# Performance work log

Measured on AMD Instinct MI355X. Metric: run time of the kernel, lower is better.

The kernel has to match this reference:

```python
import jax, jax.numpy as jnp
import numpy as np

C_RGLRU = 8.0

def _rg_lru(x, wa, ba, wx, bx, lam):
    # x: [B, L, D]. Griffin RG-LRU (De et al. 2024).
    r = jax.nn.sigmoid(jnp.einsum('bld,ed->ble', x, wa) + ba)
    i = jax.nn.sigmoid(jnp.einsum('bld,ed->ble', x, wx) + bx)
    log_a = -C_RGLRU * r * jax.nn.softplus(lam)          # [B,L,D], <= 0
    a = jnp.exp(log_a)
    mult = jnp.sqrt(jnp.maximum(1.0 - jnp.exp(2.0 * log_a), 0.0))
    b = mult * (i * x)
    def combine(c1, c2):
        a1, b1 = c1
        a2, b2 = c2
        return a1 * a2, a2 * b1 + b2
    _, h = jax.lax.associative_scan(combine, (a, b), axis=1)
    return h

def setup_inputs() -> dict:
    key = jax.random.key(0)
    ks = jax.random.split(key, 12)
    B, L, D, R = 4, 2048, 2048, 2560
    s_d = 1.0 / np.sqrt(D)
    s_r = 1.0 / np.sqrt(R)
    s_c = 1.0 / np.sqrt(R * 4)
    return {
        'x':      jax.random.normal(ks[0], (B, L, D), jnp.float32),
        'w1':     jax.random.normal(ks[1], (R, D), jnp.float32) * s_d,
        'b1':     jnp.zeros((R,), jnp.float32),
        'conv_w': jax.random.normal(ks[2], (R, R, 4), jnp.float32) * s_c,
        'conv_b': jnp.zeros((R,), jnp.float32),
        'wa':     jax.random.normal(ks[3], (R, R), jnp.float32) * s_r,
        'ba':     jnp.zeros((R,), jnp.float32),
        'wx':     jax.random.normal(ks[4], (R, R), jnp.float32) * s_r,
        'bx':     jnp.zeros((R,), jnp.float32),
        'lam':    jax.random.uniform(ks[5], (R,), jnp.float32, 0.5, 2.0),
        'w2':     jax.random.normal(ks[6], (D, R), jnp.float32) * s_r,
        'b2':     jnp.zeros((D,), jnp.float32),
    }

def reference(x, w1, b1, conv_w, conv_b, wa, ba, wx, bx, lam, w2, b2):
    # linear1 + SiLU: [B,L,D] -> [B,L,R]
    h = jax.nn.silu(jnp.einsum('bld,rd->blr', x, w1) + b1)
    # temporal conv1d: kernel 4, dilation 2, padding 3 both sides (as in torch)
    hc = h.transpose(0, 2, 1)  # [B,R,L]
    hc = jax.lax.conv_general_dilated(
        hc, conv_w, window_strides=(1,), padding=[(3, 3)],
        rhs_dilation=(2,), dimension_numbers=('NCH', 'OIH', 'NCH'))
    hc = hc + conv_b[None, :, None]
    h = hc.transpose(0, 2, 1)  # [B,L,R]
    # RG-LRU gated linear recurrence
    h = _rg_lru(h, wa, ba, wx, bx, lam)
    # linear2: [B,L,R] -> [B,L,D]
    return jnp.einsum('blr,dr->bld', h, w2) + b2
```

## Files before the change

kernel.cpp:

```cpp
#include <hip/hip_runtime.h>

#define B_  4
#define L_  2048
#define D_  2048
#define R_  2560
#define BL_ (B_ * L_)
#define LP_ (L_ + 6)

#define CHK_  16
#define CLEN_ (L_ / CHK_)

typedef unsigned short u16;
typedef unsigned int   u32;

typedef __attribute__((ext_vector_type(8))) short short8;
typedef __attribute__((ext_vector_type(4))) float f32x4;

static __device__ __forceinline__ u16 f2bf(float f) {
  u32 x = __float_as_uint(f);
  x += 0x7fffu + ((x >> 16) & 1u);
  return (u16)(x >> 16);
}
static __device__ __forceinline__ float bf2f(u16 u) {
  return __uint_as_float(((u32)u) << 16);
}

static __device__ __forceinline__ void gld16(const u16* g, u16* l) {
  __builtin_amdgcn_global_load_lds(
      (const __attribute__((address_space(1))) void*)g,
      (__attribute__((address_space(3))) void*)l, 16, 0, 0);
}

#define SB0()     __builtin_amdgcn_sched_barrier(0)
#define BAR()     __builtin_amdgcn_s_barrier()
#define LGKM0()   do { asm volatile("s_waitcnt lgkmcnt(0)" ::: "memory"); SB0(); } while (0)

__global__ void cvt_bf16(const float* __restrict__ src, u16* __restrict__ dst, int n) {
  int i = blockIdx.x * blockDim.x + threadIdx.x;
  int stride = gridDim.x * blockDim.x;
  for (; i < n; i += stride) dst[i] = f2bf(src[i]);
}

__global__ void cvt_convw(const float* __restrict__ cw, u16* __restrict__ out) {
  int i = blockIdx.x * blockDim.x + threadIdx.x;
  if (i >= R_ * R_) return;
  const float4 v = *(const float4*)(cw + (size_t)i * 4);
  out[(size_t)0 * R_ * R_ + i] = f2bf(v.x);
  out[(size_t)1 * R_ * R_ + i] = f2bf(v.y);
  out[(size_t)2 * R_ * R_ + i] = f2bf(v.z);
  out[(size_t)3 * R_ * R_ + i] = f2bf(v.w);
}

__global__ void zero_pads(u16* __restrict__ h1p) {
  int i = blockIdx.x * blockDim.x + threadIdx.x;
  if (i >= 24 * R_) return;
  const int rr = i / R_, c = i % R_;
  const int b = rr / 6, k = rr % 6;
  const int row = b * LP_ + (k < 3 ? k : L_ + k);
  h1p[(size_t)row * R_ + c] = 0;
}

__global__ void cat_bias(const float* __restrict__ ba, const float* __restrict__ bx,
                         float* __restrict__ bcat) {
  int i = blockIdx.x * blockDim.x + threadIdx.x;
  if (i < R_) bcat[i] = ba[i];
  else if (i < 2 * R_) bcat[i] = bx[i - R_];
}

template <int NF, int IB>
__device__ __forceinline__ void mfma_block(f32x4 (&acc)[8][NF], const short8 (&aF)[4],
                                           const short8 (&bF)[NF]) {
#pragma unroll
  for (int i = 0; i < 4; ++i)
#pragma unroll
    for (int j = 0; j < NF; ++j)
      acc[IB + i][j] =
          __builtin_amdgcn_mfma_f32_16x16x32_bf16(aF[i], bF[j], acc[IB + i][j], 0, 0, 0);
}

template <int KDIM, int TAPS, int ACT, int OBF16, int PADOUT>
__global__ __launch_bounds__(512)
__attribute__((amdgpu_waves_per_eu(2, 2)))
void gemm256(const u16* __restrict__ A, const u16* __restrict__ Bm,
             const float* __restrict__ bias, void* __restrict__ Cv, int N, int NBX) {
  constexpr int NF  = 4;
  constexpr int NTK = KDIM / 64;
  constexpr int NT  = NTK * TAPS;
  constexpr int BUFU16 = 16384 + NF * 4096;
  __shared__ u16 lds[2][BUFU16];

  const int cpx = gridDim.x >> 3;
  int lin = blockIdx.x;
  lin = (lin & 7) * cpx + (lin >> 3);
  const int bx = lin % NBX, by = lin / NBX;

  const int tid  = threadIdx.x;
  const int wave = tid >> 6, lane = tid & 63;
  const int wr = wave >> 2, wc = wave & 3;
  const int q = lane >> 4, r16 = lane & 15;
  const int rsw = r16 & 7;
  const int bm = bx * 256, bn = by * 256;
  const int srow = tid >> 3;
  const int schunk = (tid & 7) ^ (srow & 7);
  const int bbatch = bm >> 11;
  const int arow0 = (TAPS == 4) ? (bm + 3 + 6 * bbatch) : bm;

  f32x4 acc[8][NF] = {};

  auto stA = [&](int u, int h) {
    const int uc = (u < NT) ? u : (NT - 1);
    const int tap = uc / NTK;
    const int ku  = (uc % NTK) * 64;
    const int sh  = (TAPS == 4) ? (2 * tap - 3) : 0;
    const u16* src = A + (size_t)(arow0 + sh + h * 128) * KDIM + ku + schunk * 8;
    u16* dst = &lds[u & 1][h * 8192 + wave * 512];
#pragma unroll
    for (int s = 0; s < 2; ++s)
      gld16(src + (size_t)(s * 64 + srow) * KDIM, dst + s * 4096);
  };
  auto stB = [&](int u, int j) {
    const int uc = (u < NT) ? u : (NT - 1);
    const int tap = uc / NTK;
    const int ku  = (uc % NTK) * 64;
    const u16* src = Bm + (size_t)tap * R_ * R_ +
                     (size_t)(bn + j * 64 + srow) * KDIM + ku + schunk * 8;
    gld16(src, &lds[u & 1][16384 + j * 4096 + wave * 512]);
  };
  auto ldA = [&](short8 (&f)[4], int p, int half, int k) {
    const int base = half * 8192 + (wr * 64 + r16) * 64 + ((k * 4 + q) ^ rsw) * 8;
#pragma unroll
    for (int i = 0; i < 4; ++i)
      f[i] = *(const short8*)&lds[p][base + i * 1024];
  };
  auto ldB = [&](short8 (&f)[NF], int p, int k) {
    const int base = 16384 + (wc * 16 + r16) * 64 + ((k * 4 + q) ^ rsw) * 8;
#pragma unroll
    for (int j = 0; j < NF; ++j)
      f[j] = *(const short8*)&lds[p][base + j * 4096];
  };

  stA(0, 0); stA(0, 1);
#pragma unroll
  for (int j = 0; j < NF; ++j) stB(0, j);
  stA(1, 0);
#pragma unroll
  for (int j = 0; j < NF; ++j) stB(1, j);
  asm volatile("s_waitcnt vmcnt(%0)" :: "n"(NF + 2) : "memory");
  SB0();
  BAR();

  short8 aF[4], bF[NF];
  for (int t = 0; t < NT; ++t) {
    const int p = t & 1;
    ldA(aF, p, 0, 0);
    ldB(bF, p, 0);
    stA(t + 1, 1);
    BAR(); LGKM0();
    __builtin_amdgcn_s_setprio(1);
    mfma_block<NF, 0>(acc, aF, bF);
    __builtin_amdgcn_s_setprio(0);
    SB0(); BAR();
    ldA(aF, p, 1, 0);
    BAR(); LGKM0();
    __builtin_amdgcn_s_setprio(1);
    mfma_block<NF, 4>(acc, aF, bF);
    __builtin_amdgcn_s_setprio(0);
    SB0(); BAR();
    ldA(aF, p, 0, 1);
    ldB(bF, p, 1);
    BAR(); LGKM0();
    __builtin_amdgcn_s_setprio(1);
    mfma_block<NF, 0>(acc, aF, bF);
    __builtin_amdgcn_s_setprio(0);
    SB0(); BAR();
    ldA(aF, p, 1, 1);
    stA(t + 2, 0);
#pragma unroll
    for (int j = 0; j < NF; ++j) stB(t + 2, j);
    BAR(); LGKM0();
    __builtin_amdgcn_s_setprio(1);
    mfma_block<NF, 4>(acc, aF, bF);
    __builtin_amdgcn_s_setprio(0);
    asm volatile("s_waitcnt vmcnt(%0)" :: "n"(NF + 2) : "memory");
    SB0(); BAR();
  }

#pragma unroll
  for (int i = 0; i < 8; ++i) {
    const int rb  = ((i & 4) ? 128 : 0) + wr * 64 + (i & 3) * 16;
    const int row = bm + rb + q * 4;
    const int orow = PADOUT ? (row + 3 + 6 * bbatch) : row;
#pragma unroll
    for (int j = 0; j < NF; ++j) {
      const int col = bn + j * 64 + wc * 16 + r16;
      const float bv = bias[col];
#pragma unroll
      for (int rr = 0; rr < 4; ++rr) {
        float v = acc[i][j][rr] + bv;
        if (ACT == 1) v = v / (1.f + __expf(-v));
        const size_t off = (size_t)(orow + rr) * N + col;
        if (OBF16) ((u16*)Cv)[off] = f2bf(v);
        else       ((float*)Cv)[off] = v;
      }
    }
  }
}

static __device__ __forceinline__ void gate_math(u16 ga_, u16 gi_, u16 h2_, float sp,
                                                 float& a, float& b) {
  const float ga = bf2f(ga_);
  const float gi = bf2f(gi_);
  const float h2 = bf2f(h2_);
  const float rr = 1.f / (1.f + __expf(-ga));
  const float ii = 1.f / (1.f + __expf(-gi));
  const float log_a = -8.f * rr * sp;
  a = __expf(log_a);
  const float e2 = __expf(2.f * log_a);
  b = sqrtf(fmaxf(1.f - e2, 0.f)) * ii * h2;
}

__global__ void scan_pass1(const u16* __restrict__ gcat, const u16* __restrict__ h2b,
                           const float* __restrict__ lam,
                           float* __restrict__ Aprod, float* __restrict__ Hend) {
  int t = blockIdx.x * blockDim.x + threadIdx.x;
  if (t >= CHK_ * B_ * R_) return;
  const int c = t / (B_ * R_), br = t % (B_ * R_);
  const int b = br / R_, r = br % R_;
  const float sp = log1pf(__expf(lam[r]));
  size_t rowbase = (size_t)b * L_ + (size_t)c * CLEN_;
  const u16* pg  = gcat + rowbase * (2 * R_) + r;
  const u16* ph2 = h2b + rowbase * R_ + r;
  float Ap = 1.f, h = 0.f;
  for (int l = 0; l < CLEN_; ++l) {
    float a, bb;
    gate_math(pg[0], pg[R_], ph2[0], sp, a, bb);
    Ap *= a;
    h = a * h + bb;
    pg += 2 * R_;
    ph2 += R_;
  }
  Aprod[t] = Ap;
  Hend[t]  = h;
}

__global__ void scan_pass2(const float* __restrict__ Aprod, float* __restrict__ Hend) {
  int br = blockIdx.x * blockDim.x + threadIdx.x;
  if (br >= B_ * R_) return;
  float h = Hend[br];
  for (int c = 1; c < CHK_; ++c) {
    const int i = c * (B_ * R_) + br;
    h = Hend[i] + Aprod[i] * h;
    Hend[i] = h;
  }
}

__global__ void scan_pass3(const u16* __restrict__ gcat, const u16* __restrict__ h2b,
                           const float* __restrict__ lam,
                           const float* __restrict__ Hend, u16* __restrict__ hs) {
  int t = blockIdx.x * blockDim.x + threadIdx.x;
  if (t >= CHK_ * B_ * R_) return;
  const int c = t / (B_ * R_), br = t % (B_ * R_);
  const int b = br / R_, r = br % R_;
  const float sp = log1pf(__expf(lam[r]));
  float h = (c == 0) ? 0.f : Hend[(size_t)(c - 1) * (B_ * R_) + br];
  size_t rowbase = (size_t)b * L_ + (size_t)c * CLEN_;
  const u16* pg  = gcat + rowbase * (2 * R_) + r;
  const u16* ph2 = h2b + rowbase * R_ + r;
  u16* po = hs + rowbase * R_ + r;
  for (int l = 0; l < CLEN_; ++l) {
    float a, bb;
    gate_math(pg[0], pg[R_], ph2[0], sp, a, bb);
    h = a * h + bb;
    *po = f2bf(h);
    pg += 2 * R_;
    ph2 += R_;
    po += R_;
  }
}

extern "C" void kernel_launch(void* const* d_in, const int* in_sizes, int n_in,
                              void* d_out, int out_size, void* d_ws, size_t ws_size,
                              hipStream_t stream) {
  (void)in_sizes; (void)n_in; (void)out_size; (void)ws_size;
  const float* x   = (const float*)d_in[0];
  const float* w1  = (const float*)d_in[1];
  const float* b1  = (const float*)d_in[2];
  const float* cw  = (const float*)d_in[3];
  const float* cb  = (const float*)d_in[4];
  const float* wa  = (const float*)d_in[5];
  const float* ba  = (const float*)d_in[6];
  const float* wx  = (const float*)d_in[7];
  const float* bx  = (const float*)d_in[8];
  const float* lam = (const float*)d_in[9];
  const float* w2  = (const float*)d_in[10];
  const float* b2  = (const float*)d_in[11];

  char* ws = (char*)d_ws;
  size_t o = 0;
  auto alloc = [&](size_t bytes) { char* p = ws + o; o += (bytes + 255) & ~255ull; return p; };

  u16* w2b   = (u16*)alloc((size_t)D_ * R_ * 2);
  u16* wcatb = (u16*)alloc((size_t)2 * R_ * R_ * 2);
  float* bcat = (float*)alloc((size_t)2 * R_ * 4);
  char* hsp = ws + o;
  u16* xb  = (u16*)alloc((size_t)BL_ * D_ * 2);
  u16* w1b = (u16*)alloc((size_t)R_ * D_ * 2);
  u16* cwb = (u16*)alloc((size_t)4 * R_ * R_ * 2);
  u16* h1p = (u16*)alloc((size_t)B_ * LP_ * R_ * 2);
  u16* h2b = (u16*)alloc((size_t)BL_ * R_ * 2);
  u16* gcat = (u16*)alloc((size_t)BL_ * 2 * R_ * 2);
  float* Aprod = (float*)alloc((size_t)CHK_ * B_ * R_ * 4);
  float* Hend  = (float*)alloc((size_t)CHK_ * B_ * R_ * 4);
  u16* hsb = (u16*)hsp;

  cvt_bf16<<<4096, 256, 0, stream>>>(x,  xb,  BL_ * D_);
  cvt_bf16<<<2048, 256, 0, stream>>>(w1, w1b, R_ * D_);
  cvt_bf16<<<2048, 256, 0, stream>>>(wa, wcatb, R_ * R_);
  cvt_bf16<<<2048, 256, 0, stream>>>(wx, wcatb + (size_t)R_ * R_, R_ * R_);
  cvt_bf16<<<2048, 256, 0, stream>>>(w2, w2b, D_ * R_);
  cvt_convw<<<(R_ * R_ + 255) / 256, 256, 0, stream>>>(cw, cwb);
  zero_pads<<<(24 * R_ + 255) / 256, 256, 0, stream>>>(h1p);
  cat_bias<<<(2 * R_ + 255) / 256, 256, 0, stream>>>(ba, bx, bcat);

  gemm256<2048, 1, 1, 1, 1><<<320, 512, 0, stream>>>(xb, w1b, b1, h1p, R_, 32);
  gemm256<2560, 4, 0, 1, 0><<<320, 512, 0, stream>>>(h1p, cwb, cb, h2b, R_, 32);
  gemm256<2560, 1, 0, 1, 0><<<640, 512, 0, stream>>>(h2b, wcatb, bcat, gcat, 2 * R_, 32);
  scan_pass1<<<(CHK_ * B_ * R_ + 255) / 256, 256, 0, stream>>>(gcat, h2b, lam, Aprod, Hend);
  scan_pass2<<<(B_ * R_ + 255) / 256, 256, 0, stream>>>(Aprod, Hend);
  scan_pass3<<<(CHK_ * B_ * R_ + 255) / 256, 256, 0, stream>>>(gcat, h2b, lam, Hend, hsb);
  gemm256<2560, 1, 0, 0, 0><<<256, 512, 0, stream>>>(hsb, w2b, b2, d_out, D_, 32);
}
```

Baseline: 1.347 ms.

## Shrink GEMM tiles from 256x256 to 128x128 with 4-wave blocks

```diff
diff --git a/kernel.cpp b/kernel.cpp
--- a/kernel.cpp
+++ b/kernel.cpp
@@ -67,26 +67,25 @@
   else if (i < 2 * R_) bcat[i] = bx[i - R_];
 }
 
-template <int NF, int IB>
-__device__ __forceinline__ void mfma_block(f32x4 (&acc)[8][NF], const short8 (&aF)[4],
-                                           const short8 (&bF)[NF]) {
-#pragma unroll
-  for (int i = 0; i < 4; ++i)
-#pragma unroll
-    for (int j = 0; j < NF; ++j)
+template <int IB>
+__device__ __forceinline__ void mfma_block(f32x4 (&acc)[4][4], const short8 (&aF)[2],
+                                           const short8 (&bF)[4]) {
+#pragma unroll
+  for (int i = 0; i < 2; ++i)
+#pragma unroll
+    for (int j = 0; j < 4; ++j)
       acc[IB + i][j] =
           __builtin_amdgcn_mfma_f32_16x16x32_bf16(aF[i], bF[j], acc[IB + i][j], 0, 0, 0);
 }
 
 template <int KDIM, int TAPS, int ACT, int OBF16, int PADOUT>
-__global__ __launch_bounds__(512)
+__global__ __launch_bounds__(256)
 __attribute__((amdgpu_waves_per_eu(2, 2)))
-void gemm256(const u16* __restrict__ A, const u16* __restrict__ Bm,
+void gemm128(const u16* __restrict__ A, const u16* __restrict__ Bm,
              const float* __restrict__ bias, void* __restrict__ Cv, int N, int NBX) {
-  constexpr int NF  = 4;
   constexpr int NTK = KDIM / 64;
   constexpr int NT  = NTK * TAPS;
-  constexpr int BUFU16 = 16384 + NF * 4096;
+  constexpr int BUFU16 = 16384;
   __shared__ u16 lds[2][BUFU16];
 
   const int cpx = gridDim.x >> 3;
@@ -96,60 +95,61 @@
 
   const int tid  = threadIdx.x;
   const int wave = tid >> 6, lane = tid & 63;
-  const int wr = wave >> 2, wc = wave & 3;
+  const int wr = wave >> 1, wc = wave & 1;
   const int q = lane >> 4, r16 = lane & 15;
   const int rsw = r16 & 7;
-  const int bm = bx * 256, bn = by * 256;
+  const int bm = bx * 128, bn = by * 128;
   const int srow = tid >> 3;
   const int schunk = (tid & 7) ^ (srow & 7);
   const int bbatch = bm >> 11;
   const int arow0 = (TAPS == 4) ? (bm + 3 + 6 * bbatch) : bm;
 
-  f32x4 acc[8][NF] = {};
+  f32x4 acc[4][4] = {};
 
   auto stA = [&](int u, int h) {
     const int uc = (u < NT) ? u : (NT - 1);
     const int tap = uc / NTK;
     const int ku  = (uc % NTK) * 64;
     const int sh  = (TAPS == 4) ? (2 * tap - 3) : 0;
-    const u16* src = A + (size_t)(arow0 + sh + h * 128) * KDIM + ku + schunk * 8;
-    u16* dst = &lds[u & 1][h * 8192 + wave * 512];
+    const u16* src = A + (size_t)(arow0 + sh + h * 64) * KDIM + ku + schunk * 8;
+    u16* dst = &lds[u & 1][h * 4096 + wave * 512];
 #pragma unroll
     for (int s = 0; s < 2; ++s)
-      gld16(src + (size_t)(s * 64 + srow) * KDIM, dst + s * 4096);
+      gld16(src + (size_t)(s * 32 + srow) * KDIM, dst + s * 2048);
   };
-  auto stB = [&](int u, int j) {
+  auto stB = [&](int u, int c) {
     const int uc = (u < NT) ? u : (NT - 1);
     const int tap = uc / NTK;
     const int ku  = (uc % NTK) * 64;
     const u16* src = Bm + (size_t)tap * R_ * R_ +
-                     (size_t)(bn + j * 64 + srow) * KDIM + ku + schunk * 8;
-    gld16(src, &lds[u & 1][16384 + j * 4096 + wave * 512]);
+                     (size_t)(bn + c * 64) * KDIM + ku + schunk * 8;
+    u16* dst = &lds[u & 1][8192 + c * 4096 + wave * 512];
+#pragma unroll
+    for (int s = 0; s < 2; ++s)
+      gld16(src + (size_t)(s * 32 + srow) * KDIM, dst + s * 2048);
   };
-  auto ldA = [&](short8 (&f)[4], int p, int half, int k) {
-    const int base = half * 8192 + (wr * 64 + r16) * 64 + ((k * 4 + q) ^ rsw) * 8;
-#pragma unroll
-    for (int i = 0; i < 4; ++i)
+  auto ldA = [&](short8 (&f)[2], int p, int half, int k) {
+    const int base = half * 4096 + (wr * 32 + r16) * 64 + ((k * 4 + q) ^ rsw) * 8;
+#pragma unroll
+    for (int i = 0; i < 2; ++i)
       f[i] = *(const short8*)&lds[p][base + i * 1024];
   };
-  auto ldB = [&](short8 (&f)[NF], int p, int k) {
-    const int base = 16384 + (wc * 16 + r16) * 64 + ((k * 4 + q) ^ rsw) * 8;
-#pragma unroll
-    for (int j = 0; j < NF; ++j)
-      f[j] = *(const short8*)&lds[p][base + j * 4096];
+  auto ldB = [&](short8 (&f)[4], int p, int k) {
+    const int base = 8192 + wc * 4096 + r16 * 64 + ((k * 4 + q) ^ rsw) * 8;
+#pragma unroll
+    for (int j = 0; j < 4; ++j)
+      f[j] = *(const short8*)&lds[p][base + j * 1024];
   };
 
   stA(0, 0); stA(0, 1);
-#pragma unroll
-  for (int j = 0; j < NF; ++j) stB(0, j);
+  stB(0, 0); stB(0, 1);
   stA(1, 0);
-#pragma unroll
-  for (int j = 0; j < NF; ++j) stB(1, j);
-  asm volatile("s_waitcnt vmcnt(%0)" :: "n"(NF + 2) : "memory");
+  stB(1, 0); stB(1, 1);
+  asm volatile("s_waitcnt vmcnt(6)" ::: "memory");
   SB0();
   BAR();
 
-  short8 aF[4], bF[NF];
+  short8 aF[2], bF[4];
   for (int t = 0; t < NT; ++t) {
     const int p = t & 1;
     ldA(aF, p, 0, 0);
@@ -157,46 +157,44 @@
     stA(t + 1, 1);
     BAR(); LGKM0();
     __builtin_amdgcn_s_setprio(1);
-    mfma_block<NF, 0>(acc, aF, bF);
+    mfma_block<0>(acc, aF, bF);
     __builtin_amdgcn_s_setprio(0);
     SB0(); BAR();
     ldA(aF, p, 1, 0);
     BAR(); LGKM0();
     __builtin_amdgcn_s_setprio(1);
-    mfma_block<NF, 4>(acc, aF, bF);
+    mfma_block<2>(acc, aF, bF);
     __builtin_amdgcn_s_setprio(0);
     SB0(); BAR();
     ldA(aF, p, 0, 1);
     ldB(bF, p, 1);
     BAR(); LGKM0();
     __builtin_amdgcn_s_setprio(1);
-    mfma_block<NF, 0>(acc, aF, bF);
+    mfma_block<0>(acc, aF, bF);
     __builtin_amdgcn_s_setprio(0);
     SB0(); BAR();
     ldA(aF, p, 1, 1);
     stA(t + 2, 0);
-#pragma unroll
-    for (int j = 0; j < NF; ++j) stB(t + 2, j);
+    stB(t + 2, 0); stB(t + 2, 1);
     BAR(); LGKM0();
     __builtin_amdgcn_s_setprio(1);
-    mfma_block<NF, 4>(acc, aF, bF);
+    mfma_block<2>(acc, aF, bF);
     __builtin_amdgcn_s_setprio(0);
-    asm volatile("s_waitcnt vmcnt(%0)" :: "n"(NF + 2) : "memory");
+    asm volatile("s_waitcnt vmcnt(6)" ::: "memory");
     SB0(); BAR();
   }
 
 #pragma unroll
-  for (int i = 0; i < 8; ++i) {
-    const int rb  = ((i & 4) ? 128 : 0) + wr * 64 + (i & 3) * 16;
-    const int row = bm + rb + q * 4;
+  for (int ai = 0; ai < 4; ++ai) {
+    const int row = bm + (ai >> 1) * 64 + wr * 32 + (ai & 1) * 16 + q * 4;
     const int orow = PADOUT ? (row + 3 + 6 * bbatch) : row;
 #pragma unroll
-    for (int j = 0; j < NF; ++j) {
-      const int col = bn + j * 64 + wc * 16 + r16;
+    for (int j = 0; j < 4; ++j) {
+      const int col = bn + wc * 64 + j * 16 + r16;
       const float bv = bias[col];
 #pragma unroll
       for (int rr = 0; rr < 4; ++rr) {
-        float v = acc[i][j][rr] + bv;
+        float v = acc[ai][j][rr] + bv;
         if (ACT == 1) v = v / (1.f + __expf(-v));
         const size_t off = (size_t)(orow + rr) * N + col;
         if (OBF16) ((u16*)Cv)[off] = f2bf(v);
@@ -322,11 +320,11 @@
   zero_pads<<<(24 * R_ + 255) / 256, 256, 0, stream>>>(h1p);
   cat_bias<<<(2 * R_ + 255) / 256, 256, 0, stream>>>(ba, bx, bcat);
 
-  gemm256<2048, 1, 1, 1, 1><<<320, 512, 0, stream>>>(xb, w1b, b1, h1p, R_, 32);
-  gemm256<2560, 4, 0, 1, 0><<<320, 512, 0, stream>>>(h1p, cwb, cb, h2b, R_, 32);
-  gemm256<2560, 1, 0, 1, 0><<<640, 512, 0, stream>>>(h2b, wcatb, bcat, gcat, 2 * R_, 32);
+  gemm128<2048, 1, 1, 1, 1><<<1280, 256, 0, stream>>>(xb, w1b, b1, h1p, R_, 64);
+  gemm128<2560, 4, 0, 1, 0><<<1280, 256, 0, stream>>>(h1p, cwb, cb, h2b, R_, 64);
+  gemm128<2560, 1, 0, 1, 0><<<2560, 256, 0, stream>>>(h2b, wcatb, bcat, gcat, 2 * R_, 64);
   scan_pass1<<<(CHK_ * B_ * R_ + 255) / 256, 256, 0, stream>>>(gcat, h2b, lam, Aprod, Hend);
   scan_pass2<<<(B_ * R_ + 255) / 256, 256, 0, stream>>>(Aprod, Hend);
   scan_pass3<<<(CHK_ * B_ * R_ + 255) / 256, 256, 0, stream>>>(gcat, h2b, lam, Hend, hsb);
-  gemm256<2560, 1, 0, 0, 0><<<256, 512, 0, stream>>>(hsb, w2b, b2, d_out, D_, 32);
-}
+  gemm128<2560, 1, 0, 0, 0><<<1024, 256, 0, stream>>>(hsb, w2b, b2, d_out, D_, 64);
+}
```

Result: slower. 1.392 ms (+3.3%).
